# Kernel tuning notes

Hardware: AMD Instinct MI355X
Metric: run time of the kernel (lower is better)

## Reference

```python
import jax, jax.numpy as jnp
import numpy as np

C = 128          # inchannel
CH = C // 2      # projected channels
N_, D_, H_, W_ = 2, 16, 16, 16


def setup_inputs() -> dict:
    key = jax.random.key(0)
    kx, kq, kk, kv, kp = jax.random.split(key, 5)
    s_in = 1.0 / np.sqrt(C)
    s_mid = 1.0 / np.sqrt(CH)
    return {
        "x": jax.random.normal(kx, (N_, C, D_, H_, W_), dtype=jnp.float32),
        "Wq": jax.random.normal(kq, (CH, C), dtype=jnp.float32) * s_in,
        "Wk": jax.random.normal(kk, (CH, C), dtype=jnp.float32) * s_in,
        "Wv": jax.random.normal(kv, (CH, C), dtype=jnp.float32) * s_in,
        "Wpost": jax.random.normal(kp, (C, CH), dtype=jnp.float32) * s_mid,
    }


def reference(x, Wq, Wk, Wv, Wpost):
    n, c_in, d, h, w = x.shape
    npos = d * h * w
    xf = x.reshape(n, c_in, npos)                     # (n, C, N)
    # 1x1x1 conv3d (no bias) == channel-mixing matmul
    q = jnp.einsum('oc,ncx->nox', Wq, xf)             # (n, CH, N)
    k = jnp.einsum('oc,ncx->nox', Wk, xf)             # (n, CH, N)
    v = jnp.einsum('oc,ncx->nox', Wv, xf)             # (n, CH, N)
    # atten_map[b,i,j] = sum_c k[b,c,i] * q[b,c,j], softmax over j (dim=2)
    scores = jnp.einsum('nci,ncj->nij', k, q)         # (n, N, N)
    attn = jax.nn.softmax(scores, axis=2)
    # val @ attn: out[b,c,j] = sum_i v[b,c,i] * attn[b,i,j]
    agg = jnp.einsum('nci,nij->ncj', v, attn)         # (n, CH, N)
    post = jnp.einsum('oc,ncx->nox', Wpost, agg)      # (n, C, N)
    return post.reshape(n, c_in, d, h, w) + x
```

## Files before the change

kernel.cpp:

```cpp
#include <hip/hip_runtime.h>
#include <math.h>

#define NB   2
#define CIN  128
#define CH   64
#define NPOS 4096

typedef __attribute__((ext_vector_type(8))) short s16x8;
typedef __attribute__((ext_vector_type(4))) float f32x4;

#define FB(b,T,kc) ((((size_t)(b) * 256 + (size_t)(T)) * 2 + (size_t)(kc)) * 512)
#define VB(b,ct,it) ((((size_t)(b) * 4 + (size_t)(ct)) * 128 + (size_t)(it)) * 512)

__device__ __forceinline__ unsigned int bfrne(float f) {
    unsigned int u = __float_as_uint(f);
    return (u + 0x7FFFu + ((u >> 16) & 1u)) >> 16;
}
__device__ __forceinline__ unsigned int pk_rne(float lo, float hi) {
    return bfrne(lo) | (bfrne(hi) << 16);
}
__device__ __forceinline__ unsigned int pk_fast(float lo, float hi) {
    unsigned int a = (__float_as_uint(lo) + 0x8000u) >> 16;
    unsigned int b = (__float_as_uint(hi) + 0x8000u) & 0xFFFF0000u;
    return a | b;
}
__device__ __forceinline__ float bf2f(unsigned short h) {
    return __uint_as_float(((unsigned int)h) << 16);
}

#define XTS 132
__global__ __launch_bounds__(256) void qkv_kernel(
    const float* __restrict__ x,
    const float* __restrict__ Wq, const float* __restrict__ Wk,
    const float* __restrict__ Wv,
    unsigned short* __restrict__ kF, unsigned short* __restrict__ qF,
    unsigned short* __restrict__ vF)
{
    __shared__ __align__(16) float xT[16 * XTS];
    const int b  = blockIdx.y;
    const int pt = blockIdx.x;
    const int p0 = pt * 16;
    const int tid = threadIdx.x;

    #pragma unroll
    for (int it = 0; it < 2; ++it) {
        int idx = it * 256 + tid;
        int c = idx >> 2, p4 = (idx & 3) * 4;
        float4 g = *(const float4*)&x[((size_t)b * CIN + c) * NPOS + p0 + p4];
        xT[(p4 + 0) * XTS + c] = g.x;
        xT[(p4 + 1) * XTS + c] = g.y;
        xT[(p4 + 2) * XTS + c] = g.z;
        xT[(p4 + 3) * XTS + c] = g.w;
    }
    __syncthreads();

    const int w = tid >> 6, l = tid & 63, lm = l & 15, lq = l >> 4;

    s16x8 Bhi[4], Blo[4];
    #pragma unroll
    for (int ck = 0; ck < 4; ++ck) {
        const float* xr = &xT[lm * XTS + ck * 32 + lq * 8];
        union { unsigned int u[4]; s16x8 v; } chv, clv;
        #pragma unroll
        for (int j = 0; j < 4; ++j) {
            float x0 = xr[2 * j], x1 = xr[2 * j + 1];
            unsigned int h0 = bfrne(x0), h1 = bfrne(x1);
            chv.u[j] = h0 | (h1 << 16);
            clv.u[j] = pk_rne(x0 - __uint_as_float(h0 << 16),
                              x1 - __uint_as_float(h1 << 16));
        }
        Bhi[ck] = chv.v; Blo[ck] = clv.v;
    }

    #pragma unroll
    for (int t3 = 0; t3 < 3; ++t3) {
        const int tile = w * 3 + t3;
        const int mat = tile >> 2, o0 = (tile & 3) * 16;
        const float* __restrict__ W = (mat == 0) ? Wq : (mat == 1) ? Wk : Wv;
        f32x4 acc = {0.f, 0.f, 0.f, 0.f};
        #pragma unroll
        for (int ck = 0; ck < 4; ++ck) {
            const float* wp = W + (o0 + lm) * CIN + ck * 32 + lq * 8;
            union { unsigned int u[4]; s16x8 v; } ca;
            #pragma unroll
            for (int j = 0; j < 4; ++j) ca.u[j] = pk_rne(wp[2*j], wp[2*j+1]);
            acc = __builtin_amdgcn_mfma_f32_16x16x32_bf16(ca.v, Bhi[ck], acc, 0,0,0);
            acc = __builtin_amdgcn_mfma_f32_16x16x32_bf16(ca.v, Blo[ck], acc, 0,0,0);
        }
        if (mat < 2) {
            unsigned short* dst = (mat == 0) ? qF : kF;
            const int kc = o0 >> 5;
            const int lane2 = lm + 16 * (((o0 & 31) >> 3) + (lq >> 1));
            uint2 st = make_uint2(pk_rne(acc[0], acc[1]), pk_rne(acc[2], acc[3]));
            *(uint2*)&dst[FB(b, pt, kc) + lane2 * 8 + (lq & 1) * 4] = st;
        } else {
            const int ct = o0 >> 4;
            const int itile = pt >> 1;
            const int lanebase = 16 * ((pt & 1) * 2 + (lm >> 3));
            #pragma unroll
            for (int r = 0; r < 4; ++r)
                vF[VB(b, ct, itile) + (size_t)(4 * lq + r + lanebase) * 8
                   + (lm & 7)] = (unsigned short)bfrne(acc[r]);
        }
    }
}

__global__ __launch_bounds__(256, 4) void stats_kernel(
    const unsigned short* __restrict__ kF,
    const unsigned short* __restrict__ qF,
    float* __restrict__ lpart)
{
    const int b  = blockIdx.z;
    const int jq = blockIdx.y;
    const int tid = threadIdx.x;
    const int w = tid >> 6, l = tid & 63, lm = l & 15, lq = l >> 4;
    const int it = blockIdx.x * 4 + w;

    s16x8 a[2][2];
    #pragma unroll
    for (int s = 0; s < 2; ++s)
        #pragma unroll
        for (int kc = 0; kc < 2; ++kc)
            a[s][kc] = *(const s16x8*)&kF[FB(b, it * 2 + s, kc) + l * 8];

    const unsigned short* q0 = qF + FB(b, jq * 32, 0);
    s16x8 nb0 = *(const s16x8*)&q0[l * 8];
    s16x8 nb1 = *(const s16x8*)&q0[512 + l * 8];

    float rs[2][4] = {};
    for (int t = 0; t < 32; ++t) {
        s16x8 b0 = nb0, b1 = nb1;
        if (t < 31) {
            nb0 = *(const s16x8*)&q0[(size_t)(t + 1) * 1024 + l * 8];
            nb1 = *(const s16x8*)&q0[(size_t)(t + 1) * 1024 + 512 + l * 8];
        }
        #pragma unroll
        for (int s = 0; s < 2; ++s) {
            f32x4 sc = {0.f, 0.f, 0.f, 0.f};
            sc = __builtin_amdgcn_mfma_f32_16x16x32_bf16(a[s][0], b0, sc, 0,0,0);
            sc = __builtin_amdgcn_mfma_f32_16x16x32_bf16(a[s][1], b1, sc, 0,0,0);
            rs[s][0] += __expf(sc[0]); rs[s][1] += __expf(sc[1]);
            rs[s][2] += __expf(sc[2]); rs[s][3] += __expf(sc[3]);
        }
    }

    #pragma unroll
    for (int s = 0; s < 2; ++s)
        #pragma unroll
        for (int r = 0; r < 4; ++r) {
            rs[s][r] += __shfl_xor(rs[s][r], 1);
            rs[s][r] += __shfl_xor(rs[s][r], 2);
            rs[s][r] += __shfl_xor(rs[s][r], 4);
            rs[s][r] += __shfl_xor(rs[s][r], 8);
        }
    if (lm == 0) {
        #pragma unroll
        for (int s = 0; s < 2; ++s)
            #pragma unroll
            for (int r = 0; r < 4; ++r)
                lpart[(size_t)jq * NB * NPOS + b * NPOS
                      + it * 32 + s * 16 + lq * 4 + r] = rs[s][r];
    }
}

__global__ __launch_bounds__(256, 3) void agg_kernel(
    const unsigned short* __restrict__ kF,
    const unsigned short* __restrict__ qF,
    const unsigned short* __restrict__ vF,
    const float* __restrict__ lpart,
    unsigned short* __restrict__ U)
{
    __shared__ __align__(16) unsigned short wts[4][16][40];
    __shared__ __align__(16) float rls[512];
    const int b  = blockIdx.z;
    const int iq = blockIdx.y;
    const int j0 = blockIdx.x * 128;
    const int tid = threadIdx.x;
    const int w = tid >> 6, l = tid & 63, lm = l & 15, lq = l >> 4;

    {
        const float* lp = lpart + (size_t)b * NPOS + iq * 512 + tid * 2;
        float s0 = 0.f, s1 = 0.f;
        #pragma unroll
        for (int qq = 0; qq < 8; ++qq) {
            float2 lv = *(const float2*)(lp + (size_t)qq * NB * NPOS);
            s0 += lv.x; s1 += lv.y;
        }
        rls[tid * 2 + 0] = 1.0f / s0;
        rls[tid * 2 + 1] = 1.0f / s1;
    }

    s16x8 qb[2][2];
    #pragma unroll
    for (int js = 0; js < 2; ++js)
        #pragma unroll
        for (int kc = 0; kc < 2; ++kc)
            qb[js][kc] = *(const s16x8*)&qF[
                FB(b, blockIdx.x * 8 + w * 2 + js, kc) + l * 8];

    f32x4 acc[2][4] = {};
    s16x8 nk[2][2], nv[4];
    #pragma unroll
    for (int s = 0; s < 2; ++s)
        #pragma unroll
        for (int kc = 0; kc < 2; ++kc)
            nk[s][kc] = *(const s16x8*)&kF[FB(b, iq * 32 + s, kc) + l * 8];
    #pragma unroll
    for (int cs = 0; cs < 4; ++cs)
        nv[cs] = *(const s16x8*)&vF[VB(b, cs, iq * 16) + l * 8];

    __syncthreads();

    for (int t = 0; t < 16; ++t) {
        s16x8 kA[2][2] = {{nk[0][0], nk[0][1]}, {nk[1][0], nk[1][1]}};
        s16x8 vA[4] = {nv[0], nv[1], nv[2], nv[3]};
        if (t < 15) {
            #pragma unroll
            for (int s = 0; s < 2; ++s)
                #pragma unroll
                for (int kc = 0; kc < 2; ++kc)
                    nk[s][kc] = *(const s16x8*)&kF[
                        FB(b, iq * 32 + (t + 1) * 2 + s, kc) + l * 8];
            #pragma unroll
            for (int cs = 0; cs < 4; ++cs)
                nv[cs] = *(const s16x8*)&vF[VB(b, cs, iq * 16 + t + 1) + l * 8];
        }

        f32x4 rl0 = *(const f32x4*)&rls[t * 32 + lq * 4];
        f32x4 rl1 = *(const f32x4*)&rls[t * 32 + 16 + lq * 4];

        #pragma unroll
        for (int js = 0; js < 2; ++js) {
            f32x4 s0 = {0,0,0,0}, s1 = {0,0,0,0};
            s0 = __builtin_amdgcn_mfma_f32_16x16x32_bf16(kA[0][0], qb[js][0], s0, 0,0,0);
            s0 = __builtin_amdgcn_mfma_f32_16x16x32_bf16(kA[0][1], qb[js][1], s0, 0,0,0);
            s1 = __builtin_amdgcn_mfma_f32_16x16x32_bf16(kA[1][0], qb[js][0], s1, 0,0,0);
            s1 = __builtin_amdgcn_mfma_f32_16x16x32_bf16(kA[1][1], qb[js][1], s1, 0,0,0);

            unsigned int P0[2], P1[2];
            P0[0] = pk_fast(__expf(s0[0]) * rl0[0], __expf(s0[1]) * rl0[1]);
            P0[1] = pk_fast(__expf(s0[2]) * rl0[2], __expf(s0[3]) * rl0[3]);
            P1[0] = pk_fast(__expf(s1[0]) * rl1[0], __expf(s1[1]) * rl1[1]);
            P1[1] = pk_fast(__expf(s1[2]) * rl1[2], __expf(s1[3]) * rl1[3]);

            *(uint2*)&wts[w][lm][4 * lq]      = make_uint2(P0[0], P0[1]);
            *(uint2*)&wts[w][lm][16 + 4 * lq] = make_uint2(P1[0], P1[1]);
            s16x8 Bv = *(const s16x8*)&wts[w][lm][8 * lq];

            #pragma unroll
            for (int cs = 0; cs < 4; ++cs)
                acc[js][cs] = __builtin_amdgcn_mfma_f32_16x16x32_bf16(
                    vA[cs], Bv, acc[js][cs], 0,0,0);
        }
    }

    unsigned short* Up = U + ((size_t)iq * NB + b) * NPOS * CH;
    #pragma unroll
    for (int js = 0; js < 2; ++js)
        #pragma unroll
        for (int cs = 0; cs < 4; ++cs) {
            uint2 st = make_uint2(pk_rne(acc[js][cs][0], acc[js][cs][1]),
                                  pk_rne(acc[js][cs][2], acc[js][cs][3]));
            *(uint2*)&Up[(size_t)(j0 + w * 32 + js * 16 + lm) * CH
                         + cs * 16 + lq * 4] = st;
        }
}

__global__ __launch_bounds__(256) void post_kernel(
    const float* __restrict__ x, const float* __restrict__ Wpost,
    const unsigned short* __restrict__ U, float* __restrict__ out)
{
    const int b  = blockIdx.y;
    const int p0 = blockIdx.x * 32;
    const int tid = threadIdx.x;
    const int w = tid >> 6, l = tid & 63, lm = l & 15, lq = l >> 4;
    const int psub = (w & 1) * 16, ohalf = w >> 1;
    const int p = p0 + psub + lm;
    const size_t PS = (size_t)NB * NPOS * CH;

    const unsigned short* u = U + ((size_t)b * NPOS + p) * CH;
    s16x8 Bf[2];
    #pragma unroll
    for (int ck = 0; ck < 2; ++ck) {
        float sv[8] = {};
        #pragma unroll
        for (int qq = 0; qq < 8; ++qq) {
            union { s16x8 v; unsigned short us[8]; } uu;
            uu.v = *(const s16x8*)(u + (size_t)qq * PS + ck * 32 + lq * 8);
            #pragma unroll
            for (int j = 0; j < 8; ++j) sv[j] += bf2f(uu.us[j]);
        }
        union { unsigned int u[4]; s16x8 v; } cb;
        #pragma unroll
        for (int j = 0; j < 4; ++j) cb.u[j] = pk_rne(sv[2*j], sv[2*j+1]);
        Bf[ck] = cb.v;
    }

    #pragma unroll
    for (int ot = 0; ot < 4; ++ot) {
        const int o0 = (ohalf * 4 + ot) * 16;
        f32x4 acc = {0.f, 0.f, 0.f, 0.f};
        #pragma unroll
        for (int ck = 0; ck < 2; ++ck) {
            const float* wp = Wpost + (o0 + lm) * CH + ck * 32 + lq * 8;
            union { unsigned int u[4]; s16x8 v; } ca;
            #pragma unroll
            for (int j = 0; j < 4; ++j) ca.u[j] = pk_rne(wp[2*j], wp[2*j+1]);
            acc = __builtin_amdgcn_mfma_f32_16x16x32_bf16(ca.v, Bf[ck], acc, 0,0,0);
        }
        #pragma unroll
        for (int r = 0; r < 4; ++r) {
            size_t gi = ((size_t)b * CIN + o0 + lq * 4 + r) * NPOS + p;
            out[gi] = x[gi] + acc[r];
        }
    }
}

extern "C" void kernel_launch(void* const* d_in, const int* in_sizes, int n_in,
                              void* d_out, int out_size, void* d_ws, size_t ws_size,
                              hipStream_t stream) {
    const float* x     = (const float*)d_in[0];
    const float* Wq    = (const float*)d_in[1];
    const float* Wk    = (const float*)d_in[2];
    const float* Wv    = (const float*)d_in[3];
    const float* Wpost = (const float*)d_in[4];
    float* out = (float*)d_out;

    unsigned short* kF = (unsigned short*)d_ws;
    unsigned short* qF = kF + (size_t)NB * NPOS * CH;
    unsigned short* vF = qF + (size_t)NB * NPOS * CH;
    float* lpart = (float*)(vF + (size_t)NB * NPOS * CH);
    unsigned short* U = (unsigned short*)(lpart + (size_t)8 * NB * NPOS);

    qkv_kernel  <<<dim3(NPOS / 16, NB),     256, 0, stream>>>(x, Wq, Wk, Wv, kF, qF, vF);
    stats_kernel<<<dim3(32, 8, NB),         256, 0, stream>>>(kF, qF, lpart);
    agg_kernel  <<<dim3(NPOS / 128, 8, NB), 256, 0, stream>>>(kF, qF, vF, lpart, U);
    post_kernel <<<dim3(NPOS / 32, NB),     256, 0, stream>>>(x, Wpost, U, out);
}
```

Baseline: 104.2 us.

## Fuse four attention stages into one persistent kernel with grid barriers

Merges the qkv, stats, aggregation and post-projection kernels into a single 512-block kernel separated by atomic-counter grid barriers, so three of the four kernel launches and their inter-kernel gaps disappear. A small init kernel pre-converts all weights to bf16 once per call and resets the barrier counters, so the fused stages load packed bf16 weights directly. The post stage is remapped to 16 positions per block. The approach depends on all 512 blocks being co-resident, since the spin barriers would deadlock otherwise. The fused kernel is also limited by whichever stage needs the most registers and LDS.

```diff
diff --git a/kernel.cpp b/kernel.cpp
--- a/kernel.cpp
+++ b/kernel.cpp
@@ -5,6 +5,7 @@
 #define CIN  128
 #define CH   64
 #define NPOS 4096
+#define NBLK 512
 
 typedef __attribute__((ext_vector_type(8))) short s16x8;
 typedef __attribute__((ext_vector_type(4))) float f32x4;
@@ -28,290 +29,301 @@
     return __uint_as_float(((unsigned int)h) << 16);
 }
 
+__device__ __forceinline__ void grid_barrier(int* cnt) {
+    __syncthreads();
+    if (threadIdx.x == 0) {
+        __hip_atomic_fetch_add(cnt, 1, __ATOMIC_ACQ_REL, __HIP_MEMORY_SCOPE_AGENT);
+        while (__hip_atomic_load(cnt, __ATOMIC_ACQUIRE, __HIP_MEMORY_SCOPE_AGENT) < NBLK)
+            __builtin_amdgcn_s_sleep(2);
+    }
+    __syncthreads();
+}
+
+__global__ __launch_bounds__(256) void init_kernel(
+    const float* __restrict__ Wq, const float* __restrict__ Wk,
+    const float* __restrict__ Wv, const float* __restrict__ Wpost,
+    unsigned short* __restrict__ Wb, int* __restrict__ cnt)
+{
+    const int gid = blockIdx.x * 256 + threadIdx.x;
+    if (gid < 4) cnt[gid] = 0;
+    const int base = gid * 4;
+    const int mat = base >> 13, off = base & 8191;
+    const float* src = (mat == 0) ? Wq : (mat == 1) ? Wk : (mat == 2) ? Wv : Wpost;
+    float4 f = *(const float4*)&src[off];
+    uint2 st = make_uint2(pk_rne(f.x, f.y), pk_rne(f.z, f.w));
+    *(uint2*)&Wb[mat * 8192 + off] = st;
+}
+
 #define XTS 132
-__global__ __launch_bounds__(256) void qkv_kernel(
-    const float* __restrict__ x,
-    const float* __restrict__ Wq, const float* __restrict__ Wk,
-    const float* __restrict__ Wv,
+__global__ __launch_bounds__(256) void fused_kernel(
+    const float* __restrict__ x, const unsigned short* __restrict__ Wb,
     unsigned short* __restrict__ kF, unsigned short* __restrict__ qF,
-    unsigned short* __restrict__ vF)
+    unsigned short* __restrict__ vF, float* __restrict__ lpart,
+    unsigned short* __restrict__ U, int* __restrict__ cnt,
+    float* __restrict__ out)
 {
-    __shared__ __align__(16) float xT[16 * XTS];
-    const int b  = blockIdx.y;
-    const int pt = blockIdx.x;
-    const int p0 = pt * 16;
-    const int tid = threadIdx.x;
-
-    #pragma unroll
-    for (int it = 0; it < 2; ++it) {
-        int idx = it * 256 + tid;
-        int c = idx >> 2, p4 = (idx & 3) * 4;
-        float4 g = *(const float4*)&x[((size_t)b * CIN + c) * NPOS + p0 + p4];
-        xT[(p4 + 0) * XTS + c] = g.x;
-        xT[(p4 + 1) * XTS + c] = g.y;
-        xT[(p4 + 2) * XTS + c] = g.z;
-        xT[(p4 + 3) * XTS + c] = g.w;
-    }
-    __syncthreads();
-
-    const int w = tid >> 6, l = tid & 63, lm = l & 15, lq = l >> 4;
-
-    s16x8 Bhi[4], Blo[4];
-    #pragma unroll
-    for (int ck = 0; ck < 4; ++ck) {
-        const float* xr = &xT[lm * XTS + ck * 32 + lq * 8];
-        union { unsigned int u[4]; s16x8 v; } chv, clv;
-        #pragma unroll
-        for (int j = 0; j < 4; ++j) {
-            float x0 = xr[2 * j], x1 = xr[2 * j + 1];
-            unsigned int h0 = bfrne(x0), h1 = bfrne(x1);
-            chv.u[j] = h0 | (h1 << 16);
-            clv.u[j] = pk_rne(x0 - __uint_as_float(h0 << 16),
-                              x1 - __uint_as_float(h1 << 16));
-        }
-        Bhi[ck] = chv.v; Blo[ck] = clv.v;
-    }
-
-    #pragma unroll
-    for (int t3 = 0; t3 < 3; ++t3) {
-        const int tile = w * 3 + t3;
-        const int mat = tile >> 2, o0 = (tile & 3) * 16;
-        const float* __restrict__ W = (mat == 0) ? Wq : (mat == 1) ? Wk : Wv;
-        f32x4 acc = {0.f, 0.f, 0.f, 0.f};
-        #pragma unroll
-        for (int ck = 0; ck < 4; ++ck) {
-            const float* wp = W + (o0 + lm) * CIN + ck * 32 + lq * 8;
-            union { unsigned int u[4]; s16x8 v; } ca;
-            #pragma unroll
-            for (int j = 0; j < 4; ++j) ca.u[j] = pk_rne(wp[2*j], wp[2*j+1]);
-            acc = __builtin_amdgcn_mfma_f32_16x16x32_bf16(ca.v, Bhi[ck], acc, 0,0,0);
-            acc = __builtin_amdgcn_mfma_f32_16x16x32_bf16(ca.v, Blo[ck], acc, 0,0,0);
-        }
-        if (mat < 2) {
-            unsigned short* dst = (mat == 0) ? qF : kF;
-            const int kc = o0 >> 5;
-            const int lane2 = lm + 16 * (((o0 & 31) >> 3) + (lq >> 1));
-            uint2 st = make_uint2(pk_rne(acc[0], acc[1]), pk_rne(acc[2], acc[3]));
-            *(uint2*)&dst[FB(b, pt, kc) + lane2 * 8 + (lq & 1) * 4] = st;
-        } else {
-            const int ct = o0 >> 4;
-            const int itile = pt >> 1;
-            const int lanebase = 16 * ((pt & 1) * 2 + (lm >> 3));
-            #pragma unroll
-            for (int r = 0; r < 4; ++r)
-                vF[VB(b, ct, itile) + (size_t)(4 * lq + r + lanebase) * 8
-                   + (lm & 7)] = (unsigned short)bfrne(acc[r]);
-        }
-    }
-}
-
-__global__ __launch_bounds__(256, 4) void stats_kernel(
-    const unsigned short* __restrict__ kF,
-    const unsigned short* __restrict__ qF,
-    float* __restrict__ lpart)
-{
-    const int b  = blockIdx.z;
-    const int jq = blockIdx.y;
+    __shared__ __align__(16) unsigned char smem[8448];
+    const int g   = blockIdx.x;
+    const int b   = g >> 8;
     const int tid = threadIdx.x;
     const int w = tid >> 6, l = tid & 63, lm = l & 15, lq = l >> 4;
-    const int it = blockIdx.x * 4 + w;
-
-    s16x8 a[2][2];
-    #pragma unroll
-    for (int s = 0; s < 2; ++s)
-        #pragma unroll
-        for (int kc = 0; kc < 2; ++kc)
-            a[s][kc] = *(const s16x8*)&kF[FB(b, it * 2 + s, kc) + l * 8];
-
-    const unsigned short* q0 = qF + FB(b, jq * 32, 0);
-    s16x8 nb0 = *(const s16x8*)&q0[l * 8];
-    s16x8 nb1 = *(const s16x8*)&q0[512 + l * 8];
-
-    float rs[2][4] = {};
-    for (int t = 0; t < 32; ++t) {
-        s16x8 b0 = nb0, b1 = nb1;
-        if (t < 31) {
-            nb0 = *(const s16x8*)&q0[(size_t)(t + 1) * 1024 + l * 8];
-            nb1 = *(const s16x8*)&q0[(size_t)(t + 1) * 1024 + 512 + l * 8];
-        }
-        #pragma unroll
-        for (int s = 0; s < 2; ++s) {
-            f32x4 sc = {0.f, 0.f, 0.f, 0.f};
-            sc = __builtin_amdgcn_mfma_f32_16x16x32_bf16(a[s][0], b0, sc, 0,0,0);
-            sc = __builtin_amdgcn_mfma_f32_16x16x32_bf16(a[s][1], b1, sc, 0,0,0);
-            rs[s][0] += __expf(sc[0]); rs[s][1] += __expf(sc[1]);
-            rs[s][2] += __expf(sc[2]); rs[s][3] += __expf(sc[3]);
-        }
-    }
-
-    #pragma unroll
-    for (int s = 0; s < 2; ++s)
-        #pragma unroll
-        for (int r = 0; r < 4; ++r) {
-            rs[s][r] += __shfl_xor(rs[s][r], 1);
-            rs[s][r] += __shfl_xor(rs[s][r], 2);
-            rs[s][r] += __shfl_xor(rs[s][r], 4);
-            rs[s][r] += __shfl_xor(rs[s][r], 8);
-        }
-    if (lm == 0) {
+
+    {
+        float* xT = (float*)smem;
+        const int pt = g & 255;
+        const int p0 = pt * 16;
+
+        #pragma unroll
+        for (int it = 0; it < 2; ++it) {
+            int idx = it * 256 + tid;
+            int c = idx >> 2, p4 = (idx & 3) * 4;
+            float4 gg = *(const float4*)&x[((size_t)b * CIN + c) * NPOS + p0 + p4];
+            xT[(p4 + 0) * XTS + c] = gg.x;
+            xT[(p4 + 1) * XTS + c] = gg.y;
+            xT[(p4 + 2) * XTS + c] = gg.z;
+            xT[(p4 + 3) * XTS + c] = gg.w;
+        }
+        __syncthreads();
+
+        s16x8 Bhi[4], Blo[4];
+        #pragma unroll
+        for (int ck = 0; ck < 4; ++ck) {
+            const float* xr = &xT[lm * XTS + ck * 32 + lq * 8];
+            union { unsigned int u[4]; s16x8 v; } chv, clv;
+            #pragma unroll
+            for (int j = 0; j < 4; ++j) {
+                float x0 = xr[2 * j], x1 = xr[2 * j + 1];
+                unsigned int h0 = bfrne(x0), h1 = bfrne(x1);
+                chv.u[j] = h0 | (h1 << 16);
+                clv.u[j] = pk_rne(x0 - __uint_as_float(h0 << 16),
+                                  x1 - __uint_as_float(h1 << 16));
+            }
+            Bhi[ck] = chv.v; Blo[ck] = clv.v;
+        }
+
+        #pragma unroll
+        for (int t3 = 0; t3 < 3; ++t3) {
+            const int tile = w * 3 + t3;
+            const int mat = tile >> 2, o0 = (tile & 3) * 16;
+            const unsigned short* Wm = Wb + mat * 8192;
+            f32x4 acc = {0.f, 0.f, 0.f, 0.f};
+            #pragma unroll
+            for (int ck = 0; ck < 4; ++ck) {
+                s16x8 aW = *(const s16x8*)&Wm[(o0 + lm) * CIN + ck * 32 + lq * 8];
+                acc = __builtin_amdgcn_mfma_f32_16x16x32_bf16(aW, Bhi[ck], acc, 0,0,0);
+                acc = __builtin_amdgcn_mfma_f32_16x16x32_bf16(aW, Blo[ck], acc, 0,0,0);
+            }
+            if (mat < 2) {
+                unsigned short* dst = (mat == 0) ? qF : kF;
+                const int kc = o0 >> 5;
+                const int lane2 = lm + 16 * (((o0 & 31) >> 3) + (lq >> 1));
+                uint2 st = make_uint2(pk_rne(acc[0], acc[1]), pk_rne(acc[2], acc[3]));
+                *(uint2*)&dst[FB(b, pt, kc) + lane2 * 8 + (lq & 1) * 4] = st;
+            } else {
+                const int ct = o0 >> 4;
+                const int itile = pt >> 1;
+                const int lanebase = 16 * ((pt & 1) * 2 + (lm >> 3));
+                #pragma unroll
+                for (int r = 0; r < 4; ++r)
+                    vF[VB(b, ct, itile) + (size_t)(4 * lq + r + lanebase) * 8
+                       + (lm & 7)] = (unsigned short)bfrne(acc[r]);
+            }
+        }
+    }
+
+    grid_barrier(&cnt[0]);
+
+    {
+        const int r2 = g & 255;
+        const int jq = r2 & 7;
+        const int it = (r2 >> 3) * 4 + w;
+
+        s16x8 a[2][2];
         #pragma unroll
         for (int s = 0; s < 2; ++s)
             #pragma unroll
-            for (int r = 0; r < 4; ++r)
-                lpart[(size_t)jq * NB * NPOS + b * NPOS
-                      + it * 32 + s * 16 + lq * 4 + r] = rs[s][r];
-    }
-}
-
-__global__ __launch_bounds__(256, 3) void agg_kernel(
-    const unsigned short* __restrict__ kF,
-    const unsigned short* __restrict__ qF,
-    const unsigned short* __restrict__ vF,
-    const float* __restrict__ lpart,
-    unsigned short* __restrict__ U)
-{
-    __shared__ __align__(16) unsigned short wts[4][16][40];
-    __shared__ __align__(16) float rls[512];
-    const int b  = blockIdx.z;
-    const int iq = blockIdx.y;
-    const int j0 = blockIdx.x * 128;
-    const int tid = threadIdx.x;
-    const int w = tid >> 6, l = tid & 63, lm = l & 15, lq = l >> 4;
+            for (int kc = 0; kc < 2; ++kc)
+                a[s][kc] = *(const s16x8*)&kF[FB(b, it * 2 + s, kc) + l * 8];
+
+        const unsigned short* q0 = qF + FB(b, jq * 32, 0);
+        s16x8 nb0 = *(const s16x8*)&q0[l * 8];
+        s16x8 nb1 = *(const s16x8*)&q0[512 + l * 8];
+
+        float rs[2][4] = {};
+        for (int t = 0; t < 32; ++t) {
+            s16x8 b0 = nb0, b1 = nb1;
+            if (t < 31) {
+                nb0 = *(const s16x8*)&q0[(size_t)(t + 1) * 1024 + l * 8];
+                nb1 = *(const s16x8*)&q0[(size_t)(t + 1) * 1024 + 512 + l * 8];
+            }
+            #pragma unroll
+            for (int s = 0; s < 2; ++s) {
+                f32x4 sc = {0.f, 0.f, 0.f, 0.f};
+                sc = __builtin_amdgcn_mfma_f32_16x16x32_bf16(a[s][0], b0, sc, 0,0,0);
+                sc = __builtin_amdgcn_mfma_f32_16x16x32_bf16(a[s][1], b1, sc, 0,0,0);
+                rs[s][0] += __expf(sc[0]); rs[s][1] += __expf(sc[1]);
+                rs[s][2] += __expf(sc[2]); rs[s][3] += __expf(sc[3]);
+            }
+        }
+
+        #pragma unroll
+        for (int s = 0; s < 2; ++s)
+            #pragma unroll
+            for (int r = 0; r < 4; ++r) {
+                rs[s][r] += __shfl_xor(rs[s][r], 1);
+                rs[s][r] += __shfl_xor(rs[s][r], 2);
+                rs[s][r] += __shfl_xor(rs[s][r], 4);
+                rs[s][r] += __shfl_xor(rs[s][r], 8);
+            }
+        if (lm == 0) {
+            #pragma unroll
+            for (int s = 0; s < 2; ++s)
+                #pragma unroll
+                for (int r = 0; r < 4; ++r)
+                    lpart[(size_t)jq * NB * NPOS + b * NPOS
+                          + it * 32 + s * 16 + lq * 4 + r] = rs[s][r];
+        }
+    }
+
+    grid_barrier(&cnt[1]);
 
     {
-        const float* lp = lpart + (size_t)b * NPOS + iq * 512 + tid * 2;
-        float s0 = 0.f, s1 = 0.f;
-        #pragma unroll
-        for (int qq = 0; qq < 8; ++qq) {
-            float2 lv = *(const float2*)(lp + (size_t)qq * NB * NPOS);
-            s0 += lv.x; s1 += lv.y;
-        }
-        rls[tid * 2 + 0] = 1.0f / s0;
-        rls[tid * 2 + 1] = 1.0f / s1;
-    }
-
-    s16x8 qb[2][2];
-    #pragma unroll
-    for (int js = 0; js < 2; ++js)
-        #pragma unroll
-        for (int kc = 0; kc < 2; ++kc)
-            qb[js][kc] = *(const s16x8*)&qF[
-                FB(b, blockIdx.x * 8 + w * 2 + js, kc) + l * 8];
-
-    f32x4 acc[2][4] = {};
-    s16x8 nk[2][2], nv[4];
-    #pragma unroll
-    for (int s = 0; s < 2; ++s)
-        #pragma unroll
-        for (int kc = 0; kc < 2; ++kc)
-            nk[s][kc] = *(const s16x8*)&kF[FB(b, iq * 32 + s, kc) + l * 8];
-    #pragma unroll
-    for (int cs = 0; cs < 4; ++cs)
-        nv[cs] = *(const s16x8*)&vF[VB(b, cs, iq * 16) + l * 8];
-
-    __syncthreads();
-
-    for (int t = 0; t < 16; ++t) {
-        s16x8 kA[2][2] = {{nk[0][0], nk[0][1]}, {nk[1][0], nk[1][1]}};
-        s16x8 vA[4] = {nv[0], nv[1], nv[2], nv[3]};
-        if (t < 15) {
-            #pragma unroll
-            for (int s = 0; s < 2; ++s)
-                #pragma unroll
-                for (int kc = 0; kc < 2; ++kc)
-                    nk[s][kc] = *(const s16x8*)&kF[
-                        FB(b, iq * 32 + (t + 1) * 2 + s, kc) + l * 8];
-            #pragma unroll
-            for (int cs = 0; cs < 4; ++cs)
-                nv[cs] = *(const s16x8*)&vF[VB(b, cs, iq * 16 + t + 1) + l * 8];
-        }
-
-        f32x4 rl0 = *(const f32x4*)&rls[t * 32 + lq * 4];
-        f32x4 rl1 = *(const f32x4*)&rls[t * 32 + 16 + lq * 4];
-
-        #pragma unroll
-        for (int js = 0; js < 2; ++js) {
-            f32x4 s0 = {0,0,0,0}, s1 = {0,0,0,0};
-            s0 = __builtin_amdgcn_mfma_f32_16x16x32_bf16(kA[0][0], qb[js][0], s0, 0,0,0);
-            s0 = __builtin_amdgcn_mfma_f32_16x16x32_bf16(kA[0][1], qb[js][1], s0, 0,0,0);
-            s1 = __builtin_amdgcn_mfma_f32_16x16x32_bf16(kA[1][0], qb[js][0], s1, 0,0,0);
-            s1 = __builtin_amdgcn_mfma_f32_16x16x32_bf16(kA[1][1], qb[js][1], s1, 0,0,0);
-
-            unsigned int P0[2], P1[2];
-            P0[0] = pk_fast(__expf(s0[0]) * rl0[0], __expf(s0[1]) * rl0[1]);
-            P0[1] = pk_fast(__expf(s0[2]) * rl0[2], __expf(s0[3]) * rl0[3]);
-            P1[0] = pk_fast(__expf(s1[0]) * rl1[0], __expf(s1[1]) * rl1[1]);
-            P1[1] = pk_fast(__expf(s1[2]) * rl1[2], __expf(s1[3]) * rl1[3]);
-
-            *(uint2*)&wts[w][lm][4 * lq]      = make_uint2(P0[0], P0[1]);
-            *(uint2*)&wts[w][lm][16 + 4 * lq] = make_uint2(P1[0], P1[1]);
-            s16x8 Bv = *(const s16x8*)&wts[w][lm][8 * lq];
-
-            #pragma unroll
-            for (int cs = 0; cs < 4; ++cs)
-                acc[js][cs] = __builtin_amdgcn_mfma_f32_16x16x32_bf16(
-                    vA[cs], Bv, acc[js][cs], 0,0,0);
-        }
-    }
-
-    unsigned short* Up = U + ((size_t)iq * NB + b) * NPOS * CH;
-    #pragma unroll
-    for (int js = 0; js < 2; ++js)
-        #pragma unroll
-        for (int cs = 0; cs < 4; ++cs) {
-            uint2 st = make_uint2(pk_rne(acc[js][cs][0], acc[js][cs][1]),
-                                  pk_rne(acc[js][cs][2], acc[js][cs][3]));
-            *(uint2*)&Up[(size_t)(j0 + w * 32 + js * 16 + lm) * CH
-                         + cs * 16 + lq * 4] = st;
-        }
-}
-
-__global__ __launch_bounds__(256) void post_kernel(
-    const float* __restrict__ x, const float* __restrict__ Wpost,
-    const unsigned short* __restrict__ U, float* __restrict__ out)
-{
-    const int b  = blockIdx.y;
-    const int p0 = blockIdx.x * 32;
-    const int tid = threadIdx.x;
-    const int w = tid >> 6, l = tid & 63, lm = l & 15, lq = l >> 4;
-    const int psub = (w & 1) * 16, ohalf = w >> 1;
-    const int p = p0 + psub + lm;
-    const size_t PS = (size_t)NB * NPOS * CH;
-
-    const unsigned short* u = U + ((size_t)b * NPOS + p) * CH;
-    s16x8 Bf[2];
-    #pragma unroll
-    for (int ck = 0; ck < 2; ++ck) {
-        float sv[8] = {};
-        #pragma unroll
-        for (int qq = 0; qq < 8; ++qq) {
-            union { s16x8 v; unsigned short us[8]; } uu;
-            uu.v = *(const s16x8*)(u + (size_t)qq * PS + ck * 32 + lq * 8);
-            #pragma unroll
-            for (int j = 0; j < 8; ++j) sv[j] += bf2f(uu.us[j]);
-        }
-        union { unsigned int u[4]; s16x8 v; } cb;
-        #pragma unroll
-        for (int j = 0; j < 4; ++j) cb.u[j] = pk_rne(sv[2*j], sv[2*j+1]);
-        Bf[ck] = cb.v;
-    }
-
-    #pragma unroll
-    for (int ot = 0; ot < 4; ++ot) {
-        const int o0 = (ohalf * 4 + ot) * 16;
-        f32x4 acc = {0.f, 0.f, 0.f, 0.f};
+        unsigned short* wts = (unsigned short*)smem;
+        float* rls = (float*)(smem + 5120);
+        const int r3 = g & 255;
+        const int iq = r3 >> 5;
+        const int jb = r3 & 31;
+        const int j0 = jb * 128;
+
+        {
+            const float* lp = lpart + (size_t)b * NPOS + iq * 512 + tid * 2;
+            float s0 = 0.f, s1 = 0.f;
+            #pragma unroll
+            for (int qq = 0; qq < 8; ++qq) {
+                float2 lv = *(const float2*)(lp + (size_t)qq * NB * NPOS);
+                s0 += lv.x; s1 += lv.y;
+            }
+            rls[tid * 2 + 0] = 1.0f / s0;
+            rls[tid * 2 + 1] = 1.0f / s1;
+        }
+
+        s16x8 qb[2][2];
+        #pragma unroll
+        for (int js = 0; js < 2; ++js)
+            #pragma unroll
+            for (int kc = 0; kc < 2; ++kc)
+                qb[js][kc] = *(const s16x8*)&qF[
+                    FB(b, jb * 8 + w * 2 + js, kc) + l * 8];
+
+        f32x4 acc[2][4] = {};
+        s16x8 nk[2][2], nv[4];
+        #pragma unroll
+        for (int s = 0; s < 2; ++s)
+            #pragma unroll
+            for (int kc = 0; kc < 2; ++kc)
+                nk[s][kc] = *(const s16x8*)&kF[FB(b, iq * 32 + s, kc) + l * 8];
+        #pragma unroll
+        for (int cs = 0; cs < 4; ++cs)
+            nv[cs] = *(const s16x8*)&vF[VB(b, cs, iq * 16) + l * 8];
+
+        __syncthreads();
+
+        for (int t = 0; t < 16; ++t) {
+            s16x8 kA[2][2] = {{nk[0][0], nk[0][1]}, {nk[1][0], nk[1][1]}};
+            s16x8 vA[4] = {nv[0], nv[1], nv[2], nv[3]};
+            if (t < 15) {
+                #pragma unroll
+                for (int s = 0; s < 2; ++s)
+                    #pragma unroll
+                    for (int kc = 0; kc < 2; ++kc)
+                        nk[s][kc] = *(const s16x8*)&kF[
+                            FB(b, iq * 32 + (t + 1) * 2 + s, kc) + l * 8];
+                #pragma unroll
+                for (int cs = 0; cs < 4; ++cs)
+                    nv[cs] = *(const s16x8*)&vF[VB(b, cs, iq * 16 + t + 1) + l * 8];
+            }
+
+            f32x4 rl0 = *(const f32x4*)&rls[t * 32 + lq * 4];
+            f32x4 rl1 = *(const f32x4*)&rls[t * 32 + 16 + lq * 4];
+
+            #pragma unroll
+            for (int js = 0; js < 2; ++js) {
+                f32x4 s0 = {0,0,0,0}, s1 = {0,0,0,0};
+                s0 = __builtin_amdgcn_mfma_f32_16x16x32_bf16(kA[0][0], qb[js][0], s0, 0,0,0);
+                s0 = __builtin_amdgcn_mfma_f32_16x16x32_bf16(kA[0][1], qb[js][1], s0, 0,0,0);
+                s1 = __builtin_amdgcn_mfma_f32_16x16x32_bf16(kA[1][0], qb[js][0], s1, 0,0,0);
+                s1 = __builtin_amdgcn_mfma_f32_16x16x32_bf16(kA[1][1], qb[js][1], s1, 0,0,0);
+
+                unsigned int P0[2], P1[2];
+                P0[0] = pk_fast(__expf(s0[0]) * rl0[0], __expf(s0[1]) * rl0[1]);
+                P0[1] = pk_fast(__expf(s0[2]) * rl0[2], __expf(s0[3]) * rl0[3]);
+                P1[0] = pk_fast(__expf(s1[0]) * rl1[0], __expf(s1[1]) * rl1[1]);
+                P1[1] = pk_fast(__expf(s1[2]) * rl1[2], __expf(s1[3]) * rl1[3]);
+
+                unsigned short* wr = wts + w * 640 + lm * 40;
+                *(uint2*)&wr[4 * lq]      = make_uint2(P0[0], P0[1]);
+                *(uint2*)&wr[16 + 4 * lq] = make_uint2(P1[0], P1[1]);
+                s16x8 Bv = *(const s16x8*)&wr[8 * lq];
+
+                #pragma unroll
+                for (int cs = 0; cs < 4; ++cs)
+                    acc[js][cs] = __builtin_amdgcn_mfma_f32_16x16x32_bf16(
+                        vA[cs], Bv, acc[js][cs], 0,0,0);
+            }
+        }
+
+        unsigned short* Up = U + ((size_t)iq * NB + b) * NPOS * CH;
+        #pragma unroll
+        for (int js = 0; js < 2; ++js)
+            #pragma unroll
+            for (int cs = 0; cs < 4; ++cs) {
+                uint2 st = make_uint2(pk_rne(acc[js][cs][0], acc[js][cs][1]),
+                                      pk_rne(acc[js][cs][2], acc[js][cs][3]));
+                *(uint2*)&Up[(size_t)(j0 + w * 32 + js * 16 + lm) * CH
+                             + cs * 16 + lq * 4] = st;
+            }
+    }
+
+    grid_barrier(&cnt[2]);
+
+    {
+        const int pt = g & 255;
+        const int p = pt * 16 + lm;
+        const size_t PS = (size_t)NB * NPOS * CH;
+
+        const unsigned short* u = U + ((size_t)b * NPOS + p) * CH;
+        const unsigned short* Wpb = Wb + 3 * 8192;
+        s16x8 Bf[2];
         #pragma unroll
         for (int ck = 0; ck < 2; ++ck) {
-            const float* wp = Wpost + (o0 + lm) * CH + ck * 32 + lq * 8;
-            union { unsigned int u[4]; s16x8 v; } ca;
-            #pragma unroll
-            for (int j = 0; j < 4; ++j) ca.u[j] = pk_rne(wp[2*j], wp[2*j+1]);
-            acc = __builtin_amdgcn_mfma_f32_16x16x32_bf16(ca.v, Bf[ck], acc, 0,0,0);
-        }
-        #pragma unroll
-        for (int r = 0; r < 4; ++r) {
-            size_t gi = ((size_t)b * CIN + o0 + lq * 4 + r) * NPOS + p;
-            out[gi] = x[gi] + acc[r];
+            float sv[8] = {};
+            #pragma unroll
+            for (int qq = 0; qq < 8; ++qq) {
+                union { s16x8 v; unsigned short us[8]; } uu;
+                uu.v = *(const s16x8*)(u + (size_t)qq * PS + ck * 32 + lq * 8);
+                #pragma unroll
+                for (int j = 0; j < 8; ++j) sv[j] += bf2f(uu.us[j]);
+            }
+            union { unsigned int u[4]; s16x8 v; } cb;
+            #pragma unroll
+            for (int j = 0; j < 4; ++j) cb.u[j] = pk_rne(sv[2*j], sv[2*j+1]);
+            Bf[ck] = cb.v;
+        }
+
+        #pragma unroll
+        for (int ot = 0; ot < 2; ++ot) {
+            const int o0 = (w * 2 + ot) * 16;
+            f32x4 acc = {0.f, 0.f, 0.f, 0.f};
+            #pragma unroll
+            for (int ck = 0; ck < 2; ++ck) {
+                s16x8 aW = *(const s16x8*)&Wpb[(o0 + lm) * CH + ck * 32 + lq * 8];
+                acc = __builtin_amdgcn_mfma_f32_16x16x32_bf16(aW, Bf[ck], acc, 0,0,0);
+            }
+            #pragma unroll
+            for (int r = 0; r < 4; ++r) {
+                size_t gi = ((size_t)b * CIN + o0 + lq * 4 + r) * NPOS + p;
+                out[gi] = x[gi] + acc[r];
+            }
         }
     }
 }
@@ -326,14 +338,15 @@
     const float* Wpost = (const float*)d_in[4];
     float* out = (float*)d_out;
 
-    unsigned short* kF = (unsigned short*)d_ws;
+    unsigned short* Wb = (unsigned short*)d_ws;
+    unsigned short* kF = Wb + 4 * 8192;
     unsigned short* qF = kF + (size_t)NB * NPOS * CH;
     unsigned short* vF = qF + (size_t)NB * NPOS * CH;
     float* lpart = (float*)(vF + (size_t)NB * NPOS * CH);
     unsigned short* U = (unsigned short*)(lpart + (size_t)8 * NB * NPOS);
-
-    qkv_kernel  <<<dim3(NPOS / 16, NB),     256, 0, stream>>>(x, Wq, Wk, Wv, kF, qF, vF);
-    stats_kernel<<<dim3(32, 8, NB),         256, 0, stream>>>(kF, qF, lpart);
-    agg_kernel  <<<dim3(NPOS / 128, 8, NB), 256, 0, stream>>>(kF, qF, vF, lpart, U);
-    post_kernel <<<dim3(NPOS / 32, NB),     256, 0, stream>>>(x, Wpost, U, out);
-}
+    int* cnt = (int*)(U + (size_t)8 * NB * NPOS * CH);
+
+    init_kernel <<<dim3(32),   256, 0, stream>>>(Wq, Wk, Wv, Wpost, Wb, cnt);
+    fused_kernel<<<dim3(NBLK), 256, 0, stream>>>(x, Wb, kF, qF, vF, lpart, U,
+                                                 cnt, out);
+}
```

Result: slower. 253.3 us (+143.2%).

## Split work across more blocks in all four kernels to raise occupancy

Applied to the files above, without the earlier changes.

Each kernel's per-block work shrinks and the grid grows. qkv and post now handle one output tile group per block via a new grid dimension. stats splits the j-range into 16 chunks instead of 8, and agg processes 64 columns per block instead of 128. Launch bounds rise to allow 4 blocks per CU. The aim is more waves in flight on a 256-CU device for these small problems, at the cost of redundant loads: x is reloaded per output group, U is re-reduced per output group, and k/v tiles are refetched per column block.

```diff
diff --git a/kernel.cpp b/kernel.cpp
--- a/kernel.cpp
+++ b/kernel.cpp
@@ -29,7 +29,7 @@
 }
 
 #define XTS 132
-__global__ __launch_bounds__(256) void qkv_kernel(
+__global__ __launch_bounds__(256, 4) void qkv_kernel(
     const float* __restrict__ x,
     const float* __restrict__ Wq, const float* __restrict__ Wk,
     const float* __restrict__ Wv,
@@ -37,7 +37,8 @@
     unsigned short* __restrict__ vF)
 {
     __shared__ __align__(16) float xT[16 * XTS];
-    const int b  = blockIdx.y;
+    const int b  = blockIdx.z;
+    const int og = blockIdx.y;
     const int pt = blockIdx.x;
     const int p0 = pt * 16;
     const int tid = threadIdx.x;
@@ -72,36 +73,33 @@
         Bhi[ck] = chv.v; Blo[ck] = clv.v;
     }
 
-    #pragma unroll
-    for (int t3 = 0; t3 < 3; ++t3) {
-        const int tile = w * 3 + t3;
-        const int mat = tile >> 2, o0 = (tile & 3) * 16;
-        const float* __restrict__ W = (mat == 0) ? Wq : (mat == 1) ? Wk : Wv;
-        f32x4 acc = {0.f, 0.f, 0.f, 0.f};
-        #pragma unroll
-        for (int ck = 0; ck < 4; ++ck) {
-            const float* wp = W + (o0 + lm) * CIN + ck * 32 + lq * 8;
-            union { unsigned int u[4]; s16x8 v; } ca;
-            #pragma unroll
-            for (int j = 0; j < 4; ++j) ca.u[j] = pk_rne(wp[2*j], wp[2*j+1]);
-            acc = __builtin_amdgcn_mfma_f32_16x16x32_bf16(ca.v, Bhi[ck], acc, 0,0,0);
-            acc = __builtin_amdgcn_mfma_f32_16x16x32_bf16(ca.v, Blo[ck], acc, 0,0,0);
-        }
-        if (mat < 2) {
-            unsigned short* dst = (mat == 0) ? qF : kF;
-            const int kc = o0 >> 5;
-            const int lane2 = lm + 16 * (((o0 & 31) >> 3) + (lq >> 1));
-            uint2 st = make_uint2(pk_rne(acc[0], acc[1]), pk_rne(acc[2], acc[3]));
-            *(uint2*)&dst[FB(b, pt, kc) + lane2 * 8 + (lq & 1) * 4] = st;
-        } else {
-            const int ct = o0 >> 4;
-            const int itile = pt >> 1;
-            const int lanebase = 16 * ((pt & 1) * 2 + (lm >> 3));
-            #pragma unroll
-            for (int r = 0; r < 4; ++r)
-                vF[VB(b, ct, itile) + (size_t)(4 * lq + r + lanebase) * 8
-                   + (lm & 7)] = (unsigned short)bfrne(acc[r]);
-        }
+    const int tile = og * 4 + w;
+    const int mat = tile >> 2, o0 = (tile & 3) * 16;
+    const float* __restrict__ W = (mat == 0) ? Wq : (mat == 1) ? Wk : Wv;
+    f32x4 acc = {0.f, 0.f, 0.f, 0.f};
+    #pragma unroll
+    for (int ck = 0; ck < 4; ++ck) {
+        const float* wp = W + (o0 + lm) * CIN + ck * 32 + lq * 8;
+        union { unsigned int u[4]; s16x8 v; } ca;
+        #pragma unroll
+        for (int j = 0; j < 4; ++j) ca.u[j] = pk_rne(wp[2*j], wp[2*j+1]);
+        acc = __builtin_amdgcn_mfma_f32_16x16x32_bf16(ca.v, Bhi[ck], acc, 0,0,0);
+        acc = __builtin_amdgcn_mfma_f32_16x16x32_bf16(ca.v, Blo[ck], acc, 0,0,0);
+    }
+    if (mat < 2) {
+        unsigned short* dst = (mat == 0) ? qF : kF;
+        const int kc = o0 >> 5;
+        const int lane2 = lm + 16 * (((o0 & 31) >> 3) + (lq >> 1));
+        uint2 st = make_uint2(pk_rne(acc[0], acc[1]), pk_rne(acc[2], acc[3]));
+        *(uint2*)&dst[FB(b, pt, kc) + lane2 * 8 + (lq & 1) * 4] = st;
+    } else {
+        const int ct = o0 >> 4;
+        const int itile = pt >> 1;
+        const int lanebase = 16 * ((pt & 1) * 2 + (lm >> 3));
+        #pragma unroll
+        for (int r = 0; r < 4; ++r)
+            vF[VB(b, ct, itile) + (size_t)(4 * lq + r + lanebase) * 8
+               + (lm & 7)] = (unsigned short)bfrne(acc[r]);
     }
 }
 
@@ -123,14 +121,14 @@
         for (int kc = 0; kc < 2; ++kc)
             a[s][kc] = *(const s16x8*)&kF[FB(b, it * 2 + s, kc) + l * 8];
 
-    const unsigned short* q0 = qF + FB(b, jq * 32, 0);
+    const unsigned short* q0 = qF + FB(b, jq * 16, 0);
     s16x8 nb0 = *(const s16x8*)&q0[l * 8];
     s16x8 nb1 = *(const s16x8*)&q0[512 + l * 8];
 
     float rs[2][4] = {};
-    for (int t = 0; t < 32; ++t) {
+    for (int t = 0; t < 16; ++t) {
         s16x8 b0 = nb0, b1 = nb1;
-        if (t < 31) {
+        if (t < 15) {
             nb0 = *(const s16x8*)&q0[(size_t)(t + 1) * 1024 + l * 8];
             nb1 = *(const s16x8*)&q0[(size_t)(t + 1) * 1024 + 512 + l * 8];
         }
@@ -163,7 +161,7 @@
     }
 }
 
-__global__ __launch_bounds__(256, 3) void agg_kernel(
+__global__ __launch_bounds__(256, 4) void agg_kernel(
     const unsigned short* __restrict__ kF,
     const unsigned short* __restrict__ qF,
     const unsigned short* __restrict__ vF,
@@ -174,7 +172,8 @@
     __shared__ __align__(16) float rls[512];
     const int b  = blockIdx.z;
     const int iq = blockIdx.y;
-    const int j0 = blockIdx.x * 128;
+    const int jb = blockIdx.x;
+    const int j0 = jb * 64;
     const int tid = threadIdx.x;
     const int w = tid >> 6, l = tid & 63, lm = l & 15, lq = l >> 4;
 
@@ -182,7 +181,7 @@
         const float* lp = lpart + (size_t)b * NPOS + iq * 512 + tid * 2;
         float s0 = 0.f, s1 = 0.f;
         #pragma unroll
-        for (int qq = 0; qq < 8; ++qq) {
+        for (int qq = 0; qq < 16; ++qq) {
             float2 lv = *(const float2*)(lp + (size_t)qq * NB * NPOS);
             s0 += lv.x; s1 += lv.y;
         }
@@ -190,15 +189,12 @@
         rls[tid * 2 + 1] = 1.0f / s1;
     }
 
-    s16x8 qb[2][2];
-    #pragma unroll
-    for (int js = 0; js < 2; ++js)
-        #pragma unroll
-        for (int kc = 0; kc < 2; ++kc)
-            qb[js][kc] = *(const s16x8*)&qF[
-                FB(b, blockIdx.x * 8 + w * 2 + js, kc) + l * 8];
-
-    f32x4 acc[2][4] = {};
+    s16x8 qb[2];
+    #pragma unroll
+    for (int kc = 0; kc < 2; ++kc)
+        qb[kc] = *(const s16x8*)&qF[FB(b, jb * 4 + w, kc) + l * 8];
+
+    f32x4 acc[4] = {};
     s16x8 nk[2][2], nv[4];
     #pragma unroll
     for (int s = 0; s < 2; ++s)
@@ -212,8 +208,8 @@
     __syncthreads();
 
     for (int t = 0; t < 16; ++t) {
-        s16x8 kA[2][2] = {{nk[0][0], nk[0][1]}, {nk[1][0], nk[1][1]}};
-        s16x8 vA[4] = {nv[0], nv[1], nv[2], nv[3]};
+        s16x8 k00 = nk[0][0], k01 = nk[0][1], k10 = nk[1][0], k11 = nk[1][1];
+        s16x8 v0 = nv[0], v1 = nv[1], v2 = nv[2], v3 = nv[3];
         if (t < 15) {
             #pragma unroll
             for (int s = 0; s < 2; ++s)
@@ -229,53 +225,48 @@
         f32x4 rl0 = *(const f32x4*)&rls[t * 32 + lq * 4];
         f32x4 rl1 = *(const f32x4*)&rls[t * 32 + 16 + lq * 4];
 
-        #pragma unroll
-        for (int js = 0; js < 2; ++js) {
-            f32x4 s0 = {0,0,0,0}, s1 = {0,0,0,0};
-            s0 = __builtin_amdgcn_mfma_f32_16x16x32_bf16(kA[0][0], qb[js][0], s0, 0,0,0);
-            s0 = __builtin_amdgcn_mfma_f32_16x16x32_bf16(kA[0][1], qb[js][1], s0, 0,0,0);
-            s1 = __builtin_amdgcn_mfma_f32_16x16x32_bf16(kA[1][0], qb[js][0], s1, 0,0,0);
-            s1 = __builtin_amdgcn_mfma_f32_16x16x32_bf16(kA[1][1], qb[js][1], s1, 0,0,0);
-
-            unsigned int P0[2], P1[2];
-            P0[0] = pk_fast(__expf(s0[0]) * rl0[0], __expf(s0[1]) * rl0[1]);
-            P0[1] = pk_fast(__expf(s0[2]) * rl0[2], __expf(s0[3]) * rl0[3]);
-            P1[0] = pk_fast(__expf(s1[0]) * rl1[0], __expf(s1[1]) * rl1[1]);
-            P1[1] = pk_fast(__expf(s1[2]) * rl1[2], __expf(s1[3]) * rl1[3]);
-
-            *(uint2*)&wts[w][lm][4 * lq]      = make_uint2(P0[0], P0[1]);
-            *(uint2*)&wts[w][lm][16 + 4 * lq] = make_uint2(P1[0], P1[1]);
-            s16x8 Bv = *(const s16x8*)&wts[w][lm][8 * lq];
-
-            #pragma unroll
-            for (int cs = 0; cs < 4; ++cs)
-                acc[js][cs] = __builtin_amdgcn_mfma_f32_16x16x32_bf16(
-                    vA[cs], Bv, acc[js][cs], 0,0,0);
-        }
+        f32x4 s0 = {0,0,0,0}, s1 = {0,0,0,0};
+        s0 = __builtin_amdgcn_mfma_f32_16x16x32_bf16(k00, qb[0], s0, 0,0,0);
+        s0 = __builtin_amdgcn_mfma_f32_16x16x32_bf16(k01, qb[1], s0, 0,0,0);
+        s1 = __builtin_amdgcn_mfma_f32_16x16x32_bf16(k10, qb[0], s1, 0,0,0);
+        s1 = __builtin_amdgcn_mfma_f32_16x16x32_bf16(k11, qb[1], s1, 0,0,0);
+
+        unsigned int P0[2], P1[2];
+        P0[0] = pk_fast(__expf(s0[0]) * rl0[0], __expf(s0[1]) * rl0[1]);
+        P0[1] = pk_fast(__expf(s0[2]) * rl0[2], __expf(s0[3]) * rl0[3]);
+        P1[0] = pk_fast(__expf(s1[0]) * rl1[0], __expf(s1[1]) * rl1[1]);
+        P1[1] = pk_fast(__expf(s1[2]) * rl1[2], __expf(s1[3]) * rl1[3]);
+
+        unsigned short* wr = &wts[w][lm][0];
+        *(uint2*)&wr[4 * lq]      = make_uint2(P0[0], P0[1]);
+        *(uint2*)&wr[16 + 4 * lq] = make_uint2(P1[0], P1[1]);
+        s16x8 Bv = *(const s16x8*)&wr[8 * lq];
+
+        #pragma unroll
+        for (int cs = 0; cs < 4; ++cs)
+            acc[cs] = __builtin_amdgcn_mfma_f32_16x16x32_bf16(
+                v0, Bv, acc[cs], 0,0,0), v0 = (cs == 0) ? v1 : (cs == 1) ? v2 : v3;
     }
 
     unsigned short* Up = U + ((size_t)iq * NB + b) * NPOS * CH;
     #pragma unroll
-    for (int js = 0; js < 2; ++js)
-        #pragma unroll
-        for (int cs = 0; cs < 4; ++cs) {
-            uint2 st = make_uint2(pk_rne(acc[js][cs][0], acc[js][cs][1]),
-                                  pk_rne(acc[js][cs][2], acc[js][cs][3]));
-            *(uint2*)&Up[(size_t)(j0 + w * 32 + js * 16 + lm) * CH
-                         + cs * 16 + lq * 4] = st;
-        }
-}
-
-__global__ __launch_bounds__(256) void post_kernel(
+    for (int cs = 0; cs < 4; ++cs) {
+        uint2 st = make_uint2(pk_rne(acc[cs][0], acc[cs][1]),
+                              pk_rne(acc[cs][2], acc[cs][3]));
+        *(uint2*)&Up[(size_t)(j0 + w * 16 + lm) * CH + cs * 16 + lq * 4] = st;
+    }
+}
+
+__global__ __launch_bounds__(256, 4) void post_kernel(
     const float* __restrict__ x, const float* __restrict__ Wpost,
     const unsigned short* __restrict__ U, float* __restrict__ out)
 {
-    const int b  = blockIdx.y;
-    const int p0 = blockIdx.x * 32;
+    const int b  = blockIdx.z;
+    const int og = blockIdx.y;
+    const int p0 = blockIdx.x * 16;
     const int tid = threadIdx.x;
     const int w = tid >> 6, l = tid & 63, lm = l & 15, lq = l >> 4;
-    const int psub = (w & 1) * 16, ohalf = w >> 1;
-    const int p = p0 + psub + lm;
+    const int p = p0 + lm;
     const size_t PS = (size_t)NB * NPOS * CH;
 
     const unsigned short* u = U + ((size_t)b * NPOS + p) * CH;
@@ -296,23 +287,20 @@
         Bf[ck] = cb.v;
     }
 
-    #pragma unroll
-    for (int ot = 0; ot < 4; ++ot) {
-        const int o0 = (ohalf * 4 + ot) * 16;
-        f32x4 acc = {0.f, 0.f, 0.f, 0.f};
-        #pragma unroll
-        for (int ck = 0; ck < 2; ++ck) {
-            const float* wp = Wpost + (o0 + lm) * CH + ck * 32 + lq * 8;
-            union { unsigned int u[4]; s16x8 v; } ca;
-            #pragma unroll
-            for (int j = 0; j < 4; ++j) ca.u[j] = pk_rne(wp[2*j], wp[2*j+1]);
-            acc = __builtin_amdgcn_mfma_f32_16x16x32_bf16(ca.v, Bf[ck], acc, 0,0,0);
-        }
-        #pragma unroll
-        for (int r = 0; r < 4; ++r) {
-            size_t gi = ((size_t)b * CIN + o0 + lq * 4 + r) * NPOS + p;
-            out[gi] = x[gi] + acc[r];
-        }
+    const int o0 = (og * 4 + w) * 16;
+    f32x4 acc = {0.f, 0.f, 0.f, 0.f};
+    #pragma unroll
+    for (int ck = 0; ck < 2; ++ck) {
+        const float* wp = Wpost + (o0 + lm) * CH + ck * 32 + lq * 8;
+        union { unsigned int u[4]; s16x8 v; } ca;
+        #pragma unroll
+        for (int j = 0; j < 4; ++j) ca.u[j] = pk_rne(wp[2*j], wp[2*j+1]);
+        acc = __builtin_amdgcn_mfma_f32_16x16x32_bf16(ca.v, Bf[ck], acc, 0,0,0);
+    }
+    #pragma unroll
+    for (int r = 0; r < 4; ++r) {
+        size_t gi = ((size_t)b * CIN + o0 + lq * 4 + r) * NPOS + p;
+        out[gi] = x[gi] + acc[r];
     }
 }
 
@@ -330,10 +318,10 @@
     unsigned short* qF = kF + (size_t)NB * NPOS * CH;
     unsigned short* vF = qF + (size_t)NB * NPOS * CH;
     float* lpart = (float*)(vF + (size_t)NB * NPOS * CH);
-    unsigned short* U = (unsigned short*)(lpart + (size_t)8 * NB * NPOS);
-
-    qkv_kernel  <<<dim3(NPOS / 16, NB),     256, 0, stream>>>(x, Wq, Wk, Wv, kF, qF, vF);
-    stats_kernel<<<dim3(32, 8, NB),         256, 0, stream>>>(kF, qF, lpart);
-    agg_kernel  <<<dim3(NPOS / 128, 8, NB), 256, 0, stream>>>(kF, qF, vF, lpart, U);
-    post_kernel <<<dim3(NPOS / 32, NB),     256, 0, stream>>>(x, Wpost, U, out);
-}
+    unsigned short* U = (unsigned short*)(lpart + (size_t)16 * NB * NPOS);
+
+    qkv_kernel  <<<dim3(NPOS / 16, 3, NB), 256, 0, stream>>>(x, Wq, Wk, Wv, kF, qF, vF);
+    stats_kernel<<<dim3(32, 16, NB),       256, 0, stream>>>(kF, qF, lpart);
+    agg_kernel  <<<dim3(64, 8, NB),        256, 0, stream>>>(kF, qF, vF, lpart, U);
+    post_kernel <<<dim3(NPOS / 16, 2, NB), 256, 0, stream>>>(x, Wpost, U, out);
+}
```

Result: slower. 113.3 us (+8.7%).
